# Kernel tuning notes

Hardware: AMD Instinct MI355X
Metric: run time of the kernel (lower is better)

## Reference

```python
import jax, jax.numpy as jnp
import numpy as np

NUM_HEADS = 16


def setup_inputs() -> dict:
    key = jax.random.key(0)
    ks = jax.random.split(key, 4)
    B, S, D = 2, 2048, 1024
    scale = 1.0 / np.sqrt(D)
    x = jax.random.normal(ks[0], (B, S, D), dtype=jnp.float32)
    Wq = jax.random.normal(ks[1], (D, D), dtype=jnp.float32) * scale
    Wk = jax.random.normal(ks[2], (D, D), dtype=jnp.float32) * scale
    Wv = jax.random.normal(ks[3], (D, D), dtype=jnp.float32) * scale
    bq = jnp.zeros((D,), dtype=jnp.float32)
    bk = jnp.zeros((D,), dtype=jnp.float32)
    bv = jnp.zeros((D,), dtype=jnp.float32)
    return {"x": x, "Wq": Wq, "bq": bq, "Wk": Wk, "bk": bk, "Wv": Wv, "bv": bv}


def _split_heads(t, H):
    B, S, D = t.shape
    return t.reshape(B, S, H, D // H).transpose(0, 2, 1, 3)  # (B,H,S,depth)


def reference(x, Wq, bq, Wk, bk, Wv, bv):
    H = NUM_HEADS
    B, S, D = x.shape
    depth = D // H
    q = _split_heads(x @ Wq + bq, H)
    k = _split_heads(x @ Wk + bk, H)
    v = _split_heads(x @ Wv + bv, H)
    # causal mask: strictly-upper-triangular ones, added as finfo.min * mask
    mask = 1.0 - jnp.tril(jnp.ones((S, S), dtype=jnp.float32))
    scores = jnp.einsum("bhqd,bhkd->bhqk", q, k) / jnp.sqrt(jnp.float32(depth))
    scores = scores + jnp.float32(np.finfo(np.float32).min) * mask
    probs = jax.nn.softmax(scores, axis=-1)
    att = jnp.einsum("bhqk,bhkd->bhqd", probs, v)
    return att.transpose(0, 2, 1, 3).reshape(B, S, D)
```

## Files before the change

### kernel.cpp

```cpp
#include <hip/hip_runtime.h>
#include <hip/hip_bf16.h>

#define B_ 2
#define S_ 2048
#define D_ 1024
#define H_ 16
#define DH 64
#define M_ (B_*S_)
#define NT_ (S_/64)

using bf16x8 = __attribute__((ext_vector_type(8))) __bf16;
using f32x4  = __attribute__((ext_vector_type(4))) float;

__device__ __forceinline__ int swz(int row) { return ((row ^ (row >> 3)) & 7) << 3; }

__device__ __forceinline__ void glds16(const __bf16* g, __bf16* l) {
#if __has_builtin(__builtin_amdgcn_global_load_lds)
  __builtin_amdgcn_global_load_lds(
      (const __attribute__((address_space(1))) unsigned int*)g,
      (__attribute__((address_space(3))) unsigned int*)l, 16, 0, 0);
#else
  *(bf16x8*)l = *(const bf16x8*)g;
#endif
}

#define NBX 2048
__global__ __launch_bounds__(256) void prep(
    const float* __restrict__ x, const float* __restrict__ Wq,
    const float* __restrict__ Wk, const float* __restrict__ Wv,
    __bf16* __restrict__ xb, __bf16* __restrict__ wt) {
  int bid = blockIdx.x, tid = threadIdx.x;
  if (bid < NBX) {
    int idx = bid * 256 + tid;
    int m = idx >> 7, k = (idx & 127) * 8;
    float4 a = *(const float4*)&x[(size_t)m * D_ + k];
    float4 b = *(const float4*)&x[(size_t)m * D_ + k + 4];
    bf16x8 o;
    o[0]=(__bf16)a.x; o[1]=(__bf16)a.y; o[2]=(__bf16)a.z; o[3]=(__bf16)a.w;
    o[4]=(__bf16)b.x; o[5]=(__bf16)b.y; o[6]=(__bf16)b.z; o[7]=(__bf16)b.w;
    *(bf16x8*)&xb[(size_t)m * D_ + (k & ~63) + ((k & 63) ^ swz(m))] = o;
    return;
  }
  int wb = bid - NBX;
  int z = wb >> 8;
  int kt = (wb & 255) >> 4, nt = wb & 15;
  const float* __restrict__ W = (z == 0) ? Wq : (z == 1) ? Wk : Wv;
  __bf16* __restrict__ Wt = wt + (size_t)z * D_ * D_;
  __shared__ __bf16 Lt[64 * 66];
  int k0 = kt * 64, n0 = nt * 64;
  #pragma unroll
  for (int i = 0; i < 4; ++i) {
    int f4 = i * 256 + tid;
    int r = f4 >> 4, c4 = (f4 & 15) * 4;
    float4 v = *(const float4*)&W[(size_t)(k0 + r) * D_ + n0 + c4];
    Lt[(c4 + 0) * 66 + r] = (__bf16)v.x;
    Lt[(c4 + 1) * 66 + r] = (__bf16)v.y;
    Lt[(c4 + 2) * 66 + r] = (__bf16)v.z;
    Lt[(c4 + 3) * 66 + r] = (__bf16)v.w;
  }
  __syncthreads();
  #pragma unroll
  for (int i = 0; i < 2; ++i) {
    int idx = i * 256 + tid;
    int n = idx >> 3, kc = (idx & 7) * 8;
    int nf = n0 + n;
    bf16x8 o;
    #pragma unroll
    for (int j = 0; j < 8; ++j) o[j] = Lt[n * 66 + kc + j];
    *(bf16x8*)&Wt[(size_t)nf * D_ + k0 + (kc ^ swz(nf))] = o;
  }
}

#define BM 256
#define BN 256
#define BK 64
#define NKT (D_/BK)
#define NWG 192

__global__ __launch_bounds__(512) void qkv_gemm(
    const __bf16* __restrict__ xb, const __bf16* __restrict__ wt,
    const float* __restrict__ bq, const float* __restrict__ bk,
    const float* __restrict__ bv, __bf16* __restrict__ qk,
    __bf16* __restrict__ vt) {
  int flat = blockIdx.x;
  int sid = (flat & 7) * (NWG / 8) + (flat >> 3);
  int z = sid >> 6;
  int rem = sid & 63;
  int my = rem >> 2, nx = rem & 3;

  const __bf16* __restrict__ Wt = wt + (size_t)z * D_ * D_;
  const float* __restrict__ bias = (z == 0) ? bq : (z == 1) ? bk : bv;
  const float scale = (z == 0) ? 0.125f : 1.0f;

  __shared__ __bf16 Al[2][BM * BK];
  __shared__ __bf16 Bl[2][BM * BK];

  int tid = threadIdx.x, lane = tid & 63, w = tid >> 6;
  int m0 = my * BM, n0 = nx * BN;
  int wr = (w >> 2) * 128;
  int wc = (w & 3) * 64;

  f32x4 acc[8][4] = {};

#define STAGE(buf, kt)                                                        \
  {                                                                           \
    int k0 = (kt) * BK;                                                       \
    _Pragma("unroll")                                                         \
    for (int r = 0; r < 4; ++r) {                                             \
      int e = (r * 512 + tid) * 8;                                            \
      int row = e >> 6, col = e & 63;                                         \
      glds16(&xb[(size_t)(m0 + row) * D_ + k0 + col], &Al[buf][e]);           \
      glds16(&Wt[(size_t)(n0 + row) * D_ + k0 + col], &Bl[buf][e]);           \
    }                                                                         \
  }

  STAGE(0, 0);
  __syncthreads();

  int cur = 0;
  for (int kt = 0; kt < NKT; ++kt) {
    if (kt + 1 < NKT) STAGE(cur ^ 1, kt + 1);
    #pragma unroll
    for (int kk = 0; kk < 2; ++kk) {
      bf16x8 af[8], bfr[4];
      #pragma unroll
      for (int mi = 0; mi < 8; ++mi) {
        int row = wr + mi * 16 + (lane & 15);
        af[mi] = *(const bf16x8*)&Al[cur][row * 64 +
                 ((kk * 32 + (lane >> 4) * 8) ^ swz(row))];
      }
      #pragma unroll
      for (int ni = 0; ni < 4; ++ni) {
        int col = wc + ni * 16 + (lane & 15);
        bfr[ni] = *(const bf16x8*)&Bl[cur][col * 64 +
                  ((kk * 32 + (lane >> 4) * 8) ^ swz(col))];
      }
      #pragma unroll
      for (int mi = 0; mi < 8; ++mi)
        #pragma unroll
        for (int ni = 0; ni < 4; ++ni)
          acc[mi][ni] = __builtin_amdgcn_mfma_f32_16x16x32_bf16(
              af[mi], bfr[ni], acc[mi][ni], 0, 0, 0);
    }
    __syncthreads();
    cur ^= 1;
  }
#undef STAGE

  if (z < 2) {
    __bf16* __restrict__ out = qk + (size_t)z * M_ * D_;
    #pragma unroll
    for (int mi = 0; mi < 8; ++mi) {
      #pragma unroll
      for (int ni = 0; ni < 4; ++ni) {
        int col = n0 + wc + ni * 16 + (lane & 15);
        int h = col >> 6, dh = col & 63;
        float bv_ = bias[col];
        #pragma unroll
        for (int r = 0; r < 4; ++r) {
          int row = m0 + wr + mi * 16 + (lane >> 4) * 4 + r;
          int b = row >> 11, s = row & 2047;
          out[((size_t)(b * H_ + h) * S_ + s) * DH + dh] =
              (__bf16)((acc[mi][ni][r] + bv_) * scale);
        }
      }
    }
  } else {
    #pragma unroll
    for (int mi = 0; mi < 8; ++mi) {
      #pragma unroll
      for (int ni = 0; ni < 4; ++ni) {
        int col = n0 + wc + ni * 16 + (lane & 15);
        int h = col >> 6, dh = col & 63;
        float bv_ = bias[col];
        #pragma unroll
        for (int r = 0; r < 4; ++r) {
          int row = m0 + wr + mi * 16 + (lane >> 4) * 4 + r;
          int b = row >> 11, s = row & 2047;
          vt[((size_t)(b * H_ + h) * DH + dh) * S_ + s] =
              (__bf16)(acc[mi][ni][r] + bv_);
        }
      }
    }
  }
}

__device__ __forceinline__ void attn_tile_sw(
    const bf16x8* aq, f32x4* accO, float& m_reg, float& l_reg,
    const __bf16* __restrict__ Kl, const __bf16* __restrict__ Vt,
    __bf16* __restrict__ Plw, int lane, int kv0, int qbase, bool diag) {
  const int g = lane >> 4;
  const int ql = lane & 15;
  f32x4 sfT[4];
  __builtin_amdgcn_s_setprio(1);
  #pragma unroll
  for (int f = 0; f < 4; ++f) {
    f32x4 zz = {};
    int row = f * 16 + ql;
    int sr = swz(row);
    #pragma unroll
    for (int kk = 0; kk < 2; ++kk) {
      bf16x8 ka = *(const bf16x8*)&Kl[row * 64 + ((kk * 32 + g * 8) ^ sr)];
      zz = __builtin_amdgcn_mfma_f32_16x16x32_bf16(ka, aq[kk], zz, 0, 0, 0);
    }
    sfT[f] = zz;
  }
  __builtin_amdgcn_s_setprio(0);

  if (diag) {
    int qg = qbase + ql;
    #pragma unroll
    for (int f = 0; f < 4; ++f)
      #pragma unroll
      for (int r = 0; r < 4; ++r)
        if (kv0 + f * 16 + g * 4 + r > qg) sfT[f][r] = -1e30f;
  }

  float mx = sfT[0][0];
  #pragma unroll
  for (int f = 0; f < 4; ++f)
    #pragma unroll
    for (int r = 0; r < 4; ++r) mx = fmaxf(mx, sfT[f][r]);
  mx = fmaxf(mx, __shfl_xor(mx, 16, 64));
  mx = fmaxf(mx, __shfl_xor(mx, 32, 64));
  float mnew = fmaxf(m_reg, mx);
  float alpha = __expf(m_reg - mnew);
  m_reg = mnew;
  float rs = 0.f;
  #pragma unroll
  for (int f = 0; f < 4; ++f)
    #pragma unroll
    for (int r = 0; r < 4; ++r) {
      float p = __expf(sfT[f][r] - mnew);
      sfT[f][r] = p;
      rs += p;
    }
  rs += __shfl_xor(rs, 16, 64);
  rs += __shfl_xor(rs, 32, 64);
  l_reg = l_reg * alpha + rs;

  const int key = (ql & 7) << 3;
  #pragma unroll
  for (int f = 0; f < 4; ++f)
    #pragma unroll
    for (int r = 0; r < 4; ++r)
      Plw[ql * 64 + ((f * 16 + g * 4 + r) ^ key)] = (__bf16)sfT[f][r];

  float ab[4];
  #pragma unroll
  for (int r = 0; r < 4; ++r) ab[r] = __shfl(alpha, g * 4 + r, 16);
  #pragma unroll
  for (int f = 0; f < 4; ++f)
    #pragma unroll
    for (int r = 0; r < 4; ++r) accO[f][r] *= ab[r];

  __builtin_amdgcn_s_setprio(1);
  #pragma unroll
  for (int kk = 0; kk < 2; ++kk) {
    bf16x8 pa = *(const bf16x8*)&Plw[ql * 64 + ((kk * 32 + g * 8) ^ key)];
    #pragma unroll
    for (int f = 0; f < 4; ++f) {
      int vrow = f * 16 + ql;
      bf16x8 vb = *(const bf16x8*)&Vt[vrow * 64 + ((kk * 32 + g * 8) ^ swz(vrow))];
      accO[f] = __builtin_amdgcn_mfma_f32_16x16x32_bf16(pa, vb, accO[f], 0, 0, 0);
    }
  }
  __builtin_amdgcn_s_setprio(0);
}

__device__ __forceinline__ void attn_out_sw(
    const f32x4* accO, float l_reg, float* __restrict__ out,
    int b, int h, int qbase, int lane) {
  float lr[4];
  #pragma unroll
  for (int r = 0; r < 4; ++r) lr[r] = __shfl(l_reg, (lane >> 4) * 4 + r, 16);
  #pragma unroll
  for (int f = 0; f < 4; ++f) {
    int dh = f * 16 + (lane & 15);
    #pragma unroll
    for (int r = 0; r < 4; ++r) {
      int qg = qbase + (lane >> 4) * 4 + r;
      out[((size_t)(b * S_ + qg)) * D_ + h * DH + dh] = accO[f][r] / lr[r];
    }
  }
}

__global__ __launch_bounds__(256) void attn(
    const __bf16* __restrict__ Q, const __bf16* __restrict__ K,
    const __bf16* __restrict__ VT, float* __restrict__ out) {
  __shared__ __bf16 Kl[64 * 64];
  __shared__ __bf16 Vt[64 * 64];
  __shared__ __bf16 Pl[4][16 * 64];

  int tid = threadIdx.x, lane = tid & 63, w = tid >> 6;
  int bx = blockIdx.x, h = blockIdx.y, b = blockIdx.z;
  int qA0 = bx * 64, qB0 = (NT_ - 1 - bx) * 64;
  size_t base = ((size_t)(b * H_ + h)) * S_ * DH;
  const __bf16* __restrict__ Qg = Q + base;
  const __bf16* __restrict__ Kg = K + base;
  const __bf16* __restrict__ VTg = VT + base;

  const int g = lane >> 4, ql = lane & 15;

  bf16x8 aqA[2], aqB[2];
  int qra = qA0 + w * 16 + ql, qrb = qB0 + w * 16 + ql;
  #pragma unroll
  for (int kk = 0; kk < 2; ++kk) {
    aqA[kk] = *(const bf16x8*)&Qg[(size_t)qra * DH + kk * 32 + g * 8];
    aqB[kk] = *(const bf16x8*)&Qg[(size_t)qrb * DH + kk * 32 + g * 8];
  }

  f32x4 accA[4] = {}, accB[4] = {};
  float mA = -1e30f, lA = 0.f, mB = -1e30f, lB = 0.f;

  const int ktA = bx, ktB = NT_ - 1 - bx;

  bf16x8 kreg[2], vreg[2];
  #pragma unroll
  for (int i = 0; i < 2; ++i) {
    int e = (i * 256 + tid) * 8;
    kreg[i] = *(const bf16x8*)&Kg[(size_t)(e >> 6) * DH + (e & 63)];
    vreg[i] = *(const bf16x8*)&VTg[(size_t)(e >> 6) * S_ + (e & 63)];
  }

  for (int kt = 0; kt <= ktB; ++kt) {
    int kv0 = kt * 64;
    #pragma unroll
    for (int i = 0; i < 2; ++i) {
      int e = (i * 256 + tid) * 8;
      int rrow = e >> 6, cc = e & 63;
      *(bf16x8*)&Kl[rrow * 64 + (cc ^ swz(rrow))] = kreg[i];
      *(bf16x8*)&Vt[rrow * 64 + (cc ^ swz(rrow))] = vreg[i];
    }
    __syncthreads();

    if (kt < ktB) {
      int kvn = kv0 + 64;
      #pragma unroll
      for (int i = 0; i < 2; ++i) {
        int e = (i * 256 + tid) * 8;
        kreg[i] = *(const bf16x8*)&Kg[(size_t)(kvn + (e >> 6)) * DH + (e & 63)];
        vreg[i] = *(const bf16x8*)&VTg[(size_t)(e >> 6) * S_ + kvn + (e & 63)];
      }
    }

    attn_tile_sw(aqB, accB, mB, lB, Kl, Vt, Pl[w], lane, kv0, qB0 + w * 16,
                 kt == ktB);
    if (kt <= ktA)
      attn_tile_sw(aqA, accA, mA, lA, Kl, Vt, Pl[w], lane, kv0, qA0 + w * 16,
                   kt == ktA);
    __syncthreads();
  }

  attn_out_sw(accA, lA, out, b, h, qA0 + w * 16, lane);
  attn_out_sw(accB, lB, out, b, h, qB0 + w * 16, lane);
}

extern "C" void kernel_launch(void* const* d_in, const int* in_sizes, int n_in,
                              void* d_out, int out_size, void* d_ws, size_t ws_size,
                              hipStream_t stream) {
  const float* x  = (const float*)d_in[0];
  const float* Wq = (const float*)d_in[1];
  const float* bq = (const float*)d_in[2];
  const float* Wk = (const float*)d_in[3];
  const float* bk = (const float*)d_in[4];
  const float* Wv = (const float*)d_in[5];
  const float* bv = (const float*)d_in[6];
  float* out = (float*)d_out;

  __bf16* xb  = (__bf16*)d_ws;
  __bf16* wt  = xb + (size_t)M_ * D_;
  __bf16* qkv = wt + (size_t)3 * D_ * D_;
  __bf16* wsq = qkv;
  __bf16* wsk = qkv + (size_t)M_ * D_;
  __bf16* vtg = qkv + (size_t)2 * M_ * D_;

  prep<<<NBX + 768, 256, 0, stream>>>(x, Wq, Wk, Wv, xb, wt);
  qkv_gemm<<<NWG, 512, 0, stream>>>(xb, wt, bq, bk, bv, qkv, vtg);
  attn<<<dim3(NT_ / 2, H_, B_), 256, 0, stream>>>(wsq, wsk, vtg, out);
}
```

Baseline: 183.6 us.

## Interleave QKV GEMM loads with MFMA, stage epilogue via LDS, use exp2 softmax

The QKV GEMM main loop is restructured so that next-tile global-to-LDS loads are split into four chunks interleaved with half-tile MFMA batches. It uses explicit waitcnt and barriers plus setprio around the MFMA groups. The epilogue now stages results in LDS and writes coalesced 16-byte stores for both the Q/K layout and the transposed V layout, replacing scattered 2-byte stores. The Q scale folds in log2(e) so the attention softmax can use exp2 instead of exp. The hand-written barrier and waitcnt scheduling is fragile and adds LDS traffic in the epilogue.

After: 180.5 us. About the same (-1.7%).

```diff
diff --git a/kernel.cpp b/kernel.cpp
--- a/kernel.cpp
+++ b/kernel.cpp
@@ -10,6 +10,7 @@
 #define NT_ (S_/64)
 
 using bf16x8 = __attribute__((ext_vector_type(8))) __bf16;
+using bf16x4 = __attribute__((ext_vector_type(4))) __bf16;
 using f32x4  = __attribute__((ext_vector_type(4))) float;
 
 __device__ __forceinline__ int swz(int row) { return ((row ^ (row >> 3)) & 7) << 3; }
@@ -90,97 +91,153 @@
 
   const __bf16* __restrict__ Wt = wt + (size_t)z * D_ * D_;
   const float* __restrict__ bias = (z == 0) ? bq : (z == 1) ? bk : bv;
-  const float scale = (z == 0) ? 0.125f : 1.0f;
-
-  __shared__ __bf16 Al[2][BM * BK];
-  __shared__ __bf16 Bl[2][BM * BK];
+  const float scale = (z == 0) ? 0.18033688f : 1.0f;
+
+  __shared__ __bf16 SB[4][BM * BK];
 
   int tid = threadIdx.x, lane = tid & 63, w = tid >> 6;
+  const int g = lane >> 4, ql = lane & 15;
   int m0 = my * BM, n0 = nx * BN;
   int wr = (w >> 2) * 128;
   int wc = (w & 3) * 64;
 
   f32x4 acc[8][4] = {};
-
-#define STAGE(buf, kt)                                                        \
+  bf16x8 bfr[4];
+
+#define STAGE2(buf, kt, p)                                                    \
   {                                                                           \
     int k0 = (kt) * BK;                                                       \
     _Pragma("unroll")                                                         \
-    for (int r = 0; r < 4; ++r) {                                             \
-      int e = (r * 512 + tid) * 8;                                            \
+    for (int q = 0; q < 2; ++q) {                                             \
+      int c = 2 * (p) + q;                                                    \
+      int e = ((c & 3) * 512 + tid) * 8;                                      \
       int row = e >> 6, col = e & 63;                                         \
-      glds16(&xb[(size_t)(m0 + row) * D_ + k0 + col], &Al[buf][e]);           \
-      glds16(&Wt[(size_t)(n0 + row) * D_ + k0 + col], &Bl[buf][e]);           \
+      if (c < 4) glds16(&xb[(size_t)(m0 + row) * D_ + k0 + col], &SB[buf][e]);\
+      else glds16(&Wt[(size_t)(n0 + row) * D_ + k0 + col], &SB[2 + (buf)][e]);\
     }                                                                         \
   }
 
-  STAGE(0, 0);
+#define DSB(buf, kk)                                                          \
+  {                                                                           \
+    _Pragma("unroll")                                                         \
+    for (int ni = 0; ni < 4; ++ni) {                                          \
+      int col = wc + ni * 16 + ql;                                            \
+      bfr[ni] = *(const bf16x8*)&SB[2 + (buf)][col * 64 +                     \
+                (((kk) * 32 + g * 8) ^ swz(col))];                            \
+    }                                                                         \
+  }
+
+#define DSA4(buf, kk, mh, af)                                                 \
+  {                                                                           \
+    _Pragma("unroll")                                                         \
+    for (int mi = 0; mi < 4; ++mi) {                                          \
+      int row = wr + ((mh) * 4 + mi) * 16 + ql;                               \
+      af[mi] = *(const bf16x8*)&SB[buf][row * 64 +                            \
+               (((kk) * 32 + g * 8) ^ swz(row))];                             \
+    }                                                                         \
+  }
+
+#define MFMA16(af, mh)                                                        \
+  {                                                                           \
+    __builtin_amdgcn_s_setprio(1);                                            \
+    _Pragma("unroll")                                                         \
+    for (int mi = 0; mi < 4; ++mi)                                            \
+      _Pragma("unroll")                                                       \
+      for (int ni = 0; ni < 4; ++ni)                                          \
+        acc[(mh) * 4 + mi][ni] = __builtin_amdgcn_mfma_f32_16x16x32_bf16(     \
+            af[mi], bfr[ni], acc[(mh) * 4 + mi][ni], 0, 0, 0);                \
+    __builtin_amdgcn_s_setprio(0);                                            \
+  }
+
+  #pragma unroll
+  for (int p = 0; p < 4; ++p) STAGE2(0, 0, p);
+
+  for (int t = 0; t < NKT; ++t) {
+    int cb = t & 1, nb = cb ^ 1;
+    bool pf = (t + 1 < NKT);
+    bf16x8 af[4];
+    if (pf) STAGE2(nb, t + 1, 0);
+    __builtin_amdgcn_sched_barrier(0);
+    if (pf) { asm volatile("s_waitcnt vmcnt(2)" ::: "memory"); }
+    else    { asm volatile("s_waitcnt vmcnt(0)" ::: "memory"); }
+    __builtin_amdgcn_sched_barrier(0);
+    __builtin_amdgcn_s_barrier();
+    __builtin_amdgcn_sched_barrier(0);
+    DSB(cb, 0);
+    DSA4(cb, 0, 0, af);
+    MFMA16(af, 0);
+    if (pf) STAGE2(nb, t + 1, 1);
+    DSA4(cb, 0, 1, af);
+    __builtin_amdgcn_s_barrier();
+    MFMA16(af, 1);
+    if (pf) STAGE2(nb, t + 1, 2);
+    DSB(cb, 1);
+    DSA4(cb, 1, 0, af);
+    __builtin_amdgcn_s_barrier();
+    MFMA16(af, 0);
+    if (pf) STAGE2(nb, t + 1, 3);
+    DSA4(cb, 1, 1, af);
+    __builtin_amdgcn_s_barrier();
+    MFMA16(af, 1);
+  }
   __syncthreads();
-
-  int cur = 0;
-  for (int kt = 0; kt < NKT; ++kt) {
-    if (kt + 1 < NKT) STAGE(cur ^ 1, kt + 1);
-    #pragma unroll
-    for (int kk = 0; kk < 2; ++kk) {
-      bf16x8 af[8], bfr[4];
-      #pragma unroll
-      for (int mi = 0; mi < 8; ++mi) {
-        int row = wr + mi * 16 + (lane & 15);
-        af[mi] = *(const bf16x8*)&Al[cur][row * 64 +
-                 ((kk * 32 + (lane >> 4) * 8) ^ swz(row))];
-      }
-      #pragma unroll
-      for (int ni = 0; ni < 4; ++ni) {
-        int col = wc + ni * 16 + (lane & 15);
-        bfr[ni] = *(const bf16x8*)&Bl[cur][col * 64 +
-                  ((kk * 32 + (lane >> 4) * 8) ^ swz(col))];
-      }
-      #pragma unroll
-      for (int mi = 0; mi < 8; ++mi)
-        #pragma unroll
-        for (int ni = 0; ni < 4; ++ni)
-          acc[mi][ni] = __builtin_amdgcn_mfma_f32_16x16x32_bf16(
-              af[mi], bfr[ni], acc[mi][ni], 0, 0, 0);
-    }
-    __syncthreads();
-    cur ^= 1;
-  }
-#undef STAGE
-
-  if (z < 2) {
-    __bf16* __restrict__ out = qk + (size_t)z * M_ * D_;
+#undef STAGE2
+#undef DSB
+#undef DSA4
+#undef MFMA16
+
+  __bf16* Lt = &SB[0][0];
+  const int b = m0 >> 11;
+  const int sbase = m0 & 2047;
+  if (z == 2) {
     #pragma unroll
     for (int mi = 0; mi < 8; ++mi) {
       #pragma unroll
       for (int ni = 0; ni < 4; ++ni) {
-        int col = n0 + wc + ni * 16 + (lane & 15);
-        int h = col >> 6, dh = col & 63;
-        float bv_ = bias[col];
+        int nl = wc + ni * 16 + ql;
+        int ml = wr + mi * 16 + g * 4;
+        float bv_ = bias[n0 + nl];
+        bf16x4 p4;
+        #pragma unroll
+        for (int r = 0; r < 4; ++r) p4[r] = (__bf16)(acc[mi][ni][r] + bv_);
+        *(bf16x4*)&Lt[nl * 256 + (ml ^ ((nl & 7) << 3))] = p4;
+      }
+    }
+    __syncthreads();
+    #pragma unroll
+    for (int i = 0; i < 16; ++i) {
+      int gi = i * 512 + tid;
+      int n = gi >> 5, mg = (gi & 31) * 8;
+      bf16x8 v = *(const bf16x8*)&Lt[n * 256 + (mg ^ ((n & 7) << 3))];
+      int col = n0 + n, hh = col >> 6, dh = col & 63;
+      *(bf16x8*)&vt[((size_t)(b * H_ + hh) * DH + dh) * S_ + sbase + mg] = v;
+    }
+  } else {
+    __bf16* __restrict__ out = qk + (size_t)z * M_ * D_;
+    #pragma unroll
+    for (int mi = 0; mi < 8; ++mi) {
+      #pragma unroll
+      for (int ni = 0; ni < 4; ++ni) {
+        int nl = wc + ni * 16 + ql;
+        float bv_ = bias[n0 + nl];
         #pragma unroll
         for (int r = 0; r < 4; ++r) {
-          int row = m0 + wr + mi * 16 + (lane >> 4) * 4 + r;
-          int b = row >> 11, s = row & 2047;
-          out[((size_t)(b * H_ + h) * S_ + s) * DH + dh] =
+          int ml = wr + mi * 16 + g * 4 + r;
+          Lt[ml * 256 + (nl ^ ((ml & 7) << 3))] =
               (__bf16)((acc[mi][ni][r] + bv_) * scale);
         }
       }
     }
-  } else {
-    #pragma unroll
-    for (int mi = 0; mi < 8; ++mi) {
-      #pragma unroll
-      for (int ni = 0; ni < 4; ++ni) {
-        int col = n0 + wc + ni * 16 + (lane & 15);
-        int h = col >> 6, dh = col & 63;
-        float bv_ = bias[col];
-        #pragma unroll
-        for (int r = 0; r < 4; ++r) {
-          int row = m0 + wr + mi * 16 + (lane >> 4) * 4 + r;
-          int b = row >> 11, s = row & 2047;
-          vt[((size_t)(b * H_ + h) * DH + dh) * S_ + s] =
-              (__bf16)(acc[mi][ni][r] + bv_);
-        }
-      }
+    __syncthreads();
+    #pragma unroll
+    for (int i = 0; i < 16; ++i) {
+      int gi = i * 512 + tid;
+      int ml = gi >> 5, rest = gi & 31;
+      int hh = rest >> 3, cg = (rest & 7) * 8;
+      int n = hh * 64 + cg;
+      bf16x8 v = *(const bf16x8*)&Lt[ml * 256 + (n ^ ((ml & 7) << 3))];
+      int col = n0 + n, ho = col >> 6, dh = col & 63;
+      *(bf16x8*)&out[((size_t)(b * H_ + ho) * S_ + sbase + ml) * DH + dh] = v;
     }
   }
 }
@@ -224,14 +281,14 @@
   mx = fmaxf(mx, __shfl_xor(mx, 16, 64));
   mx = fmaxf(mx, __shfl_xor(mx, 32, 64));
   float mnew = fmaxf(m_reg, mx);
-  float alpha = __expf(m_reg - mnew);
+  float alpha = exp2f(m_reg - mnew);
   m_reg = mnew;
   float rs = 0.f;
   #pragma unroll
   for (int f = 0; f < 4; ++f)
     #pragma unroll
     for (int r = 0; r < 4; ++r) {
-      float p = __expf(sfT[f][r] - mnew);
+      float p = exp2f(sfT[f][r] - mnew);
       sfT[f][r] = p;
       rs += p;
     }
```
